# Kernel optimization log

Measured on AMD Instinct MI355X. Metric: run time of the kernel, lower is better.

The kernel has to match this reference:

```python
import jax, jax.numpy as jnp
import numpy as np

IN_F = 512
OUT_F = 512

def setup_inputs() -> dict:
    key = jax.random.key(0)
    k1, k2, k3 = jax.random.split(key, 3)
    x = jax.random.normal(k1, (2, 512, IN_F), dtype=jnp.float32)
    # uniform init: a = sqrt(6 / (2 + out_features))
    a = float(np.sqrt(6.0 / (2.0 + OUT_F)))
    W = jax.random.uniform(k2, (OUT_F, IN_F), dtype=jnp.float32, minval=-a, maxval=a)
    bound = float(1.0 / np.sqrt(IN_F))
    b = jax.random.uniform(k3, (OUT_F,), dtype=jnp.float32, minval=-bound, maxval=bound)
    return {"x": x, "W": W, "b": b}

def reference(x, W, b):
    # MAM fully connected (beta == 0 path): for each (row, out-neuron),
    # C = max_k(x_k * w_ok) + min_k(x_k * w_ok), then add bias.
    xf = x.reshape(-1, x.shape[-1])            # (B, in)
    prod = xf[:, None, :] * W[None, :, :]      # (B, out, in) -- the large intermediate
    C = prod.max(axis=-1) + prod.min(axis=-1)  # (B, out)
    C = C + b[None, :]
    return C.reshape(x.shape[:-1] + (W.shape[0],))
```

## Files before the change

### kernel.cpp

```cpp
#include <hip/hip_runtime.h>
#include <math.h>


#define O_TOTAL 512
#define K_TOTAL 512
#define OBLK 64
#define RPB 8
#define NWAVE 4
#define KQ (K_TOTAL / NWAVE)
#define KCH 32

__global__ __launch_bounds__(256, 4)
void mam_fc_kernel(const float* __restrict__ x, const float* __restrict__ W,
                   const float* __restrict__ bias, float* __restrict__ out) {
  const int lane = threadIdx.x & 63;
  const int wv = __builtin_amdgcn_readfirstlane((int)(threadIdx.x >> 6));
  const int blk = blockIdx.x;
  const int ob = blk & 7;
  const int rg = blk >> 3;
  const int o = ob * OBLK + lane;
  const int row0 = rg * RPB;
  const int k0 = wv * KQ;

  float amax[RPB], amin[RPB];
#pragma unroll
  for (int r = 0; r < RPB; ++r) { amax[r] = -INFINITY; amin[r] = INFINITY; }

  const float* Wo = W + (size_t)o * K_TOTAL + k0;

#pragma unroll
  for (int kc = 0; kc < KQ; kc += KCH) {
    float w[KCH];
#pragma unroll
    for (int j = 0; j < KCH; j += 4) {
      const float4 w4 = *reinterpret_cast<const float4*>(Wo + kc + j);
      w[j] = w4.x; w[j + 1] = w4.y; w[j + 2] = w4.z; w[j + 3] = w4.w;
    }
#pragma unroll
    for (int r = 0; r < RPB; ++r) {
      const float* xr = x + (size_t)(row0 + r) * K_TOTAL + k0 + kc;
#pragma unroll
      for (int j = 0; j < KCH; j += 4) {
        const float4 x4 = *reinterpret_cast<const float4*>(xr + j);
        const float p0 = x4.x * w[j];
        const float p1 = x4.y * w[j + 1];
        const float p2 = x4.z * w[j + 2];
        const float p3 = x4.w * w[j + 3];
        amax[r] = fmaxf(amax[r], fmaxf(p3, fmaxf(fmaxf(p0, p1), p2)));
        amin[r] = fminf(amin[r], fminf(p3, fminf(fminf(p0, p1), p2)));
      }
    }
  }

  __shared__ float redmax[NWAVE][RPB][OBLK];
  __shared__ float redmin[NWAVE][RPB][OBLK];
#pragma unroll
  for (int r = 0; r < RPB; ++r) {
    redmax[wv][r][lane] = amax[r];
    redmin[wv][r][lane] = amin[r];
  }
  __syncthreads();

  const float bv = bias[o];
#pragma unroll
  for (int rr = wv; rr < RPB; rr += NWAVE) {
    float m = redmax[0][rr][lane];
    float n = redmin[0][rr][lane];
#pragma unroll
    for (int q = 1; q < NWAVE; ++q) {
      m = fmaxf(m, redmax[q][rr][lane]);
      n = fminf(n, redmin[q][rr][lane]);
    }
    out[(size_t)(row0 + rr) * O_TOTAL + o] = m + n + bv;
  }
}

extern "C" void kernel_launch(void* const* d_in, const int* in_sizes, int n_in,
                              void* d_out, int out_size, void* d_ws, size_t ws_size,
                              hipStream_t stream) {
  const float* x = (const float*)d_in[0];
  const float* W = (const float*)d_in[1];
  const float* b = (const float*)d_in[2];
  float* out = (float*)d_out;

  const int nrows = in_sizes[0] / K_TOTAL;
  const int nblocks = (O_TOTAL / OBLK) * (nrows / RPB);
  mam_fc_kernel<<<dim3(nblocks), dim3(256), 0, stream>>>(x, W, b, out);
}
```

Baseline: 25.96 us.

## Stage W tiles in double-buffered swizzled LDS and split rows across waves

Instead of each wave reading a quarter of K straight from global memory and reducing partials through shared memory, the block now stages 64x64 W chunks in double-buffered, XOR-swizzled LDS. All four waves share each chunk, and each wave owns its own four rows over the full K range, so the cross-wave reduction is gone. Rows per block go from 8 to 16, which halves the grid to 512 blocks, and each accumulator is split into two parity chains to shorten dependency chains. The cost is a __syncthreads per chunk, a fully serial K loop per wave, and fewer blocks for the GPU's many CUs.

```diff
diff --git a/kernel.cpp b/kernel.cpp
--- a/kernel.cpp
+++ b/kernel.cpp
@@ -5,73 +5,89 @@
 #define O_TOTAL 512
 #define K_TOTAL 512
 #define OBLK 64
-#define RPB 8
 #define NWAVE 4
-#define KQ (K_TOTAL / NWAVE)
-#define KCH 32
+#define RPW 4
+#define RPB (NWAVE * RPW)
+#define KCH 64
+#define NCHUNK (K_TOTAL / KCH)
 
-__global__ __launch_bounds__(256, 4)
+__global__ __launch_bounds__(256, 2)
 void mam_fc_kernel(const float* __restrict__ x, const float* __restrict__ W,
                    const float* __restrict__ bias, float* __restrict__ out) {
-  const int lane = threadIdx.x & 63;
-  const int wv = __builtin_amdgcn_readfirstlane((int)(threadIdx.x >> 6));
-  const int blk = blockIdx.x;
-  const int ob = blk & 7;
-  const int rg = blk >> 3;
-  const int o = ob * OBLK + lane;
-  const int row0 = rg * RPB;
-  const int k0 = wv * KQ;
+  __shared__ float Wl[2][OBLK * KCH];
 
-  float amax[RPB], amin[RPB];
+  const int t = threadIdx.x;
+  const int lane = t & 63;
+  const int wv = __builtin_amdgcn_readfirstlane(t >> 6);
+  const int ob = blockIdx.x & 7;
+  const int rg = blockIdx.x >> 3;
+  const int o0 = ob * OBLK;
+  const int rowBase = rg * RPB + wv * RPW;
+
+  const int s_or = t >> 4;
+  const int s_g  = t & 15;
+
+  const float* Wg = W + (size_t)o0 * K_TOTAL;
+  const float* xr0 = x + (size_t)rowBase * K_TOTAL;
+
+  float amax[RPW][2], amin[RPW][2];
 #pragma unroll
-  for (int r = 0; r < RPB; ++r) { amax[r] = -INFINITY; amin[r] = INFINITY; }
-
-  const float* Wo = W + (size_t)o * K_TOTAL + k0;
+  for (int r = 0; r < RPW; ++r) {
+#pragma unroll
+    for (int p = 0; p < 2; ++p) { amax[r][p] = -INFINITY; amin[r][p] = INFINITY; }
+  }
 
 #pragma unroll
-  for (int kc = 0; kc < KQ; kc += KCH) {
-    float w[KCH];
-#pragma unroll
-    for (int j = 0; j < KCH; j += 4) {
-      const float4 w4 = *reinterpret_cast<const float4*>(Wo + kc + j);
-      w[j] = w4.x; w[j + 1] = w4.y; w[j + 2] = w4.z; w[j + 3] = w4.w;
-    }
-#pragma unroll
-    for (int r = 0; r < RPB; ++r) {
-      const float* xr = x + (size_t)(row0 + r) * K_TOTAL + k0 + kc;
-#pragma unroll
-      for (int j = 0; j < KCH; j += 4) {
-        const float4 x4 = *reinterpret_cast<const float4*>(xr + j);
-        const float p0 = x4.x * w[j];
-        const float p1 = x4.y * w[j + 1];
-        const float p2 = x4.z * w[j + 2];
-        const float p3 = x4.w * w[j + 3];
-        amax[r] = fmaxf(amax[r], fmaxf(p3, fmaxf(fmaxf(p0, p1), p2)));
-        amin[r] = fminf(amin[r], fminf(p3, fminf(fminf(p0, p1), p2)));
-      }
-    }
-  }
-
-  __shared__ float redmax[NWAVE][RPB][OBLK];
-  __shared__ float redmin[NWAVE][RPB][OBLK];
-#pragma unroll
-  for (int r = 0; r < RPB; ++r) {
-    redmax[wv][r][lane] = amax[r];
-    redmin[wv][r][lane] = amin[r];
+  for (int i = 0; i < 4; ++i) {
+    const int o_l = s_or + 16 * i;
+    const float4 v = *reinterpret_cast<const float4*>(Wg + (size_t)o_l * K_TOTAL + s_g * 4);
+    const int gsw = s_g ^ (o_l & 15);
+    *reinterpret_cast<float4*>(&Wl[0][o_l * KCH + gsw * 4]) = v;
   }
   __syncthreads();
 
-  const float bv = bias[o];
+#pragma unroll 1
+  for (int c = 0; c < NCHUNK; ++c) {
+    if (c + 1 < NCHUNK) {
+      const int kc2 = (c + 1) * KCH;
+      float* dst = Wl[(c + 1) & 1];
 #pragma unroll
-  for (int rr = wv; rr < RPB; rr += NWAVE) {
-    float m = redmax[0][rr][lane];
-    float n = redmin[0][rr][lane];
+      for (int i = 0; i < 4; ++i) {
+        const int o_l = s_or + 16 * i;
+        const float4 v = *reinterpret_cast<const float4*>(Wg + (size_t)o_l * K_TOTAL + kc2 + s_g * 4);
+        const int gsw = s_g ^ (o_l & 15);
+        *reinterpret_cast<float4*>(&dst[o_l * KCH + gsw * 4]) = v;
+      }
+    }
+
+    const float* buf = Wl[c & 1];
+    const int kc = c * KCH;
 #pragma unroll
-    for (int q = 1; q < NWAVE; ++q) {
-      m = fmaxf(m, redmax[q][rr][lane]);
-      n = fminf(n, redmin[q][rr][lane]);
+    for (int j = 0; j < KCH / 4; ++j) {
+      const float4 w4 = *reinterpret_cast<const float4*>(
+          &buf[lane * KCH + ((j ^ (lane & 15)) * 4)]);
+      const int par = j & 1;
+#pragma unroll
+      for (int r = 0; r < RPW; ++r) {
+        const float4 x4 = *reinterpret_cast<const float4*>(
+            xr0 + (size_t)r * K_TOTAL + kc + j * 4);
+        const float p0 = x4.x * w4.x;
+        const float p1 = x4.y * w4.y;
+        const float p2 = x4.z * w4.z;
+        const float p3 = x4.w * w4.w;
+        amax[r][par] = fmaxf(fmaxf(fmaxf(fmaxf(amax[r][par], p0), p1), p2), p3);
+        amin[r][par] = fminf(fminf(fminf(fminf(amin[r][par], p0), p1), p2), p3);
+      }
     }
-    out[(size_t)(row0 + rr) * O_TOTAL + o] = m + n + bv;
+    __syncthreads();
+  }
+
+  const float bv = bias[o0 + lane];
+#pragma unroll
+  for (int r = 0; r < RPW; ++r) {
+    const float m = fmaxf(amax[r][0], amax[r][1]);
+    const float n = fminf(amin[r][0], amin[r][1]);
+    out[(size_t)(rowBase + r) * O_TOTAL + (o0 + lane)] = m + n + bv;
   }
 }
 
```

Result: faster. 24.29 us (-6.4%).

## Transpose W into workspace and split K across eight waves per block

Applied to the files above, without the earlier changes.

Adds a pre-pass kernel that transposes W into the workspace so each wave reads W coalesced along the output dimension, with x values broadcast as scalars. Blocks grow to 512 threads, splitting K into eight segments that are reduced through shared memory. The cost is an extra kernel launch and a full write and re-read of W on every call. The per-lane float4 loads of W and x are replaced by scalar loads.

```diff
diff --git a/kernel.cpp b/kernel.cpp
--- a/kernel.cpp
+++ b/kernel.cpp
@@ -2,77 +2,96 @@
 #include <math.h>
 
 
+#define K_TOTAL 512
 #define O_TOTAL 512
-#define K_TOTAL 512
-#define OBLK 64
+#define OW 64
 #define RPB 8
-#define NWAVE 4
-#define KQ (K_TOTAL / NWAVE)
-#define KCH 32
+#define NSEG 8
+#define KSEG (K_TOTAL / NSEG)
 
-__global__ __launch_bounds__(256, 4)
-void mam_fc_kernel(const float* __restrict__ x, const float* __restrict__ W,
+__global__ __launch_bounds__(256)
+void transpose_w(const float* __restrict__ W, float* __restrict__ WT) {
+  __shared__ float tile[64][65];
+  const int t = threadIdx.x;
+  const int ob = blockIdx.x & 7;
+  const int kb = blockIdx.x >> 3;
+  const int o0 = ob * 64, k0 = kb * 64;
+#pragma unroll
+  for (int i = 0; i < 4; ++i) {
+    const int u = t + 256 * i, r = u >> 4, c = u & 15;
+    const float4 v = *reinterpret_cast<const float4*>(W + (size_t)(o0 + r) * K_TOTAL + k0 + c * 4);
+    tile[r][c * 4 + 0] = v.x; tile[r][c * 4 + 1] = v.y;
+    tile[r][c * 4 + 2] = v.z; tile[r][c * 4 + 3] = v.w;
+  }
+  __syncthreads();
+#pragma unroll
+  for (int i = 0; i < 4; ++i) {
+    const int u = t + 256 * i, kr = u >> 4, c = u & 15;
+    float4 v;
+    v.x = tile[c * 4 + 0][kr]; v.y = tile[c * 4 + 1][kr];
+    v.z = tile[c * 4 + 2][kr]; v.w = tile[c * 4 + 3][kr];
+    *reinterpret_cast<float4*>(WT + (size_t)(k0 + kr) * O_TOTAL + o0 + c * 4) = v;
+  }
+}
+
+template <bool TRANS>
+__global__ __launch_bounds__(512, 8)
+void mam_fc_kernel(const float* __restrict__ x, const float* __restrict__ Wm,
                    const float* __restrict__ bias, float* __restrict__ out) {
-  const int lane = threadIdx.x & 63;
-  const int wv = __builtin_amdgcn_readfirstlane((int)(threadIdx.x >> 6));
-  const int blk = blockIdx.x;
-  const int ob = blk & 7;
-  const int rg = blk >> 3;
-  const int o = ob * OBLK + lane;
+  __shared__ float red[NSEG][RPB][OW][2];
+
+  const int t = threadIdx.x;
+  const int lane = t & 63;
+  const int q = __builtin_amdgcn_readfirstlane(t >> 6);
+  const int ob = blockIdx.x & 7;
+  const int rg = blockIdx.x >> 3;
+  const int o0 = ob * OW;
   const int row0 = rg * RPB;
-  const int k0 = wv * KQ;
+  const int k0 = q * KSEG;
+
+  const float* xb = x + (size_t)row0 * K_TOTAL + k0;
 
   float amax[RPB], amin[RPB];
 #pragma unroll
   for (int r = 0; r < RPB; ++r) { amax[r] = -INFINITY; amin[r] = INFINITY; }
 
-  const float* Wo = W + (size_t)o * K_TOTAL + k0;
-
-#pragma unroll
-  for (int kc = 0; kc < KQ; kc += KCH) {
-    float w[KCH];
-#pragma unroll
-    for (int j = 0; j < KCH; j += 4) {
-      const float4 w4 = *reinterpret_cast<const float4*>(Wo + kc + j);
-      w[j] = w4.x; w[j + 1] = w4.y; w[j + 2] = w4.z; w[j + 3] = w4.w;
+#pragma unroll 4
+  for (int kk = 0; kk < KSEG; kk += 2) {
+    float wa, wb;
+    if (TRANS) {
+      wa = Wm[(size_t)(k0 + kk) * O_TOTAL + o0 + lane];
+      wb = Wm[(size_t)(k0 + kk + 1) * O_TOTAL + o0 + lane];
+    } else {
+      wa = Wm[(size_t)(o0 + lane) * K_TOTAL + k0 + kk];
+      wb = Wm[(size_t)(o0 + lane) * K_TOTAL + k0 + kk + 1];
     }
 #pragma unroll
     for (int r = 0; r < RPB; ++r) {
-      const float* xr = x + (size_t)(row0 + r) * K_TOTAL + k0 + kc;
-#pragma unroll
-      for (int j = 0; j < KCH; j += 4) {
-        const float4 x4 = *reinterpret_cast<const float4*>(xr + j);
-        const float p0 = x4.x * w[j];
-        const float p1 = x4.y * w[j + 1];
-        const float p2 = x4.z * w[j + 2];
-        const float p3 = x4.w * w[j + 3];
-        amax[r] = fmaxf(amax[r], fmaxf(p3, fmaxf(fmaxf(p0, p1), p2)));
-        amin[r] = fminf(amin[r], fminf(p3, fminf(fminf(p0, p1), p2)));
-      }
+      const float xa = xb[(size_t)r * K_TOTAL + kk];
+      const float xc = xb[(size_t)r * K_TOTAL + kk + 1];
+      const float pa = xa * wa;
+      const float pb = xc * wb;
+      amax[r] = fmaxf(fmaxf(amax[r], pa), pb);
+      amin[r] = fminf(fminf(amin[r], pa), pb);
     }
   }
 
-  __shared__ float redmax[NWAVE][RPB][OBLK];
-  __shared__ float redmin[NWAVE][RPB][OBLK];
 #pragma unroll
   for (int r = 0; r < RPB; ++r) {
-    redmax[wv][r][lane] = amax[r];
-    redmin[wv][r][lane] = amin[r];
+    red[q][r][lane][0] = amax[r];
+    red[q][r][lane][1] = amin[r];
   }
   __syncthreads();
 
-  const float bv = bias[o];
+  const int rr = t >> 6;
+  const int oo = t & 63;
+  float m = -INFINITY, n = INFINITY;
 #pragma unroll
-  for (int rr = wv; rr < RPB; rr += NWAVE) {
-    float m = redmax[0][rr][lane];
-    float n = redmin[0][rr][lane];
-#pragma unroll
-    for (int q = 1; q < NWAVE; ++q) {
-      m = fmaxf(m, redmax[q][rr][lane]);
-      n = fminf(n, redmin[q][rr][lane]);
-    }
-    out[(size_t)(row0 + rr) * O_TOTAL + o] = m + n + bv;
+  for (int s = 0; s < NSEG; ++s) {
+    m = fmaxf(m, red[s][rr][oo][0]);
+    n = fminf(n, red[s][rr][oo][1]);
   }
+  out[(size_t)(row0 + rr) * O_TOTAL + o0 + oo] = m + n + bias[o0 + oo];
 }
 
 extern "C" void kernel_launch(void* const* d_in, const int* in_sizes, int n_in,
@@ -84,6 +103,14 @@
   float* out = (float*)d_out;
 
   const int nrows = in_sizes[0] / K_TOTAL;
-  const int nblocks = (O_TOTAL / OBLK) * (nrows / RPB);
-  mam_fc_kernel<<<dim3(nblocks), dim3(256), 0, stream>>>(x, W, b, out);
+  const int nblocks = (O_TOTAL / OW) * (nrows / RPB);
+  const size_t wt_bytes = (size_t)K_TOTAL * O_TOTAL * sizeof(float);
+
+  if (ws_size >= wt_bytes) {
+    float* WT = (float*)d_ws;
+    transpose_w<<<dim3(64), dim3(256), 0, stream>>>(W, WT);
+    mam_fc_kernel<true><<<dim3(nblocks), dim3(512), 0, stream>>>(x, WT, b, out);
+  } else {
+    mam_fc_kernel<false><<<dim3(nblocks), dim3(512), 0, stream>>>(x, W, b, out);
+  }
 }
```

After: 24.44 us. -5.8%, faster.
